# Optimization experiments

Measured on AMD Instinct MI355X. Metric: run time of the kernel, lower is better.

## Reference

```python
import jax, jax.numpy as jnp
import numpy as np

B, S, H = 2, 2048, 1024          # batch, seq, hidden_size
I = 512                          # expert_ffn_hidden_size
E_R, E_Z = 32, 8                 # routed experts, zero (identity) experts
E_T = E_R + E_Z                  # total experts
K = 6                            # moe_topk
SCALE = 2.5                      # routed_scaling_factor
W_INIT = 0.02


def setup_inputs() -> dict:
    key = jax.random.key(0)
    k0, k1, k2, k3 = jax.random.split(key, 4)
    return {
        "hidden_states": jax.random.normal(k0, (B, S, H), jnp.float32),
        "classifier_weight": jax.random.normal(k1, (E_T, H), jnp.float32) * W_INIT,
        "e_score_correction_bias": jnp.zeros((E_T,), jnp.float32),
        "gate_up_proj": jax.random.normal(k2, (E_T, 2 * I, H), jnp.float32) * W_INIT,
        "down_proj": jax.random.normal(k3, (E_R, H, I), jnp.float32) * W_INIT,
    }


def reference(hidden_states, classifier_weight, e_score_correction_bias,
              gate_up_proj, down_proj):
    orig_shape = hidden_states.shape
    x = hidden_states.reshape(-1, H).astype(jnp.float32)      # [T, H]
    T = x.shape[0]

    # ---- router (fp32 like the torch code) ----
    logits = x @ classifier_weight.T                          # [T, E_T]
    scores = jax.nn.softmax(logits, axis=-1)
    _, topk_idx = jax.lax.top_k(scores + e_score_correction_bias[None, :], K)
    topk_w = jnp.take_along_axis(scores, topk_idx, axis=1) * SCALE  # [T, K]

    # dense per-(token, expert) combine weights; 0 for unselected experts
    w_full = jnp.zeros((T, E_T), jnp.float32).at[
        jnp.arange(T)[:, None], topk_idx].add(topk_w)          # [T, E_T]

    # zero experts: weighted identity
    zero_w = w_full[:, E_R:].sum(axis=-1, keepdims=True)       # [T, 1]
    out0 = x * zero_w

    # routed experts: SwiGLU MLP per expert, scanned over experts
    routed_w = w_full[:, :E_R].T                               # [E_R, T]

    def body(out, xs):
        Wgu, Wd, we = xs                                       # [2I,H],[H,I],[T]
        gate, up = jnp.split(x @ Wgu.T, 2, axis=-1)            # [T, I] each
        y = (jax.nn.silu(gate) * up) @ Wd.T                    # [T, H]
        return out + we[:, None] * y, None

    out, _ = jax.lax.scan(body, out0, (gate_up_proj[:E_R], down_proj, routed_w))
    return out.reshape(orig_shape).astype(hidden_states.dtype)
```

## Files before the change

### kernel.cpp

```cpp
#include <hip/hip_runtime.h>
#include <float.h>
#include <math.h>

#define TT 4096
#define HH 1024
#define II 512
#define E_R 32
#define E_T 40
#define TOPK 6
#define SCALE_F 2.5f
#define MAXTILES 224
#define NGUP (32*1024*1024)
#define NDWN (32*1024*512)

typedef __bf16 bf16x8 __attribute__((ext_vector_type(8)));
typedef float f32x4 __attribute__((ext_vector_type(4)));

__device__ inline unsigned short f2bf(float f) {
  __bf16 h = (__bf16)f;
  return __builtin_bit_cast(unsigned short, h);
}

__device__ inline bf16x8 cvt8v(float4 a, float4 b) {
  bf16x8 v;
  v[0] = (__bf16)a.x; v[1] = (__bf16)a.y; v[2] = (__bf16)a.z; v[3] = (__bf16)a.w;
  v[4] = (__bf16)b.x; v[5] = (__bf16)b.y; v[6] = (__bf16)b.z; v[7] = (__bf16)b.w;
  return v;
}

__device__ inline void gload_lds16(const void* g, void* l) {
  __builtin_amdgcn_global_load_lds(
      (__attribute__((address_space(1))) void*)g,
      (__attribute__((address_space(3))) void*)l, 16, 0, 0);
}

__device__ inline bf16x8 lds_frag(const unsigned short* base, int row, int kb) {
  int byte = (row * 128 + kb * 2) ^ ((row & 7) << 4);
  uint4 v = *reinterpret_cast<const uint4*>(reinterpret_cast<const char*>(base) + byte);
  return __builtin_bit_cast(bf16x8, v);
}

__device__ inline f32x4 mfma16(bf16x8 a, bf16x8 b, f32x4 c) {
  return __builtin_amdgcn_mfma_f32_16x16x32_bf16(a, b, c, 0, 0, 0);
}

#define WAIT_VM8()  do { asm volatile("s_waitcnt vmcnt(8)" ::: "memory"); } while (0)
#define WAIT_VM0()  do { asm volatile("s_waitcnt vmcnt(0)" ::: "memory"); } while (0)
#define SBAR()      __builtin_amdgcn_s_barrier()
#define SCHED0()    __builtin_amdgcn_sched_barrier(0)

__global__ __launch_bounds__(256) void k_convert_w(const float* __restrict__ gup,
                                                   const float* __restrict__ dwn,
                                                   uint4* __restrict__ wb) {
  unsigned i = blockIdx.x * 256 + threadIdx.x;
  const unsigned NGq = NGUP / 8;
  const float4* src = (i < NGq)
      ? reinterpret_cast<const float4*>(gup) + (size_t)i * 2
      : reinterpret_cast<const float4*>(dwn) + (size_t)(i - NGq) * 2;
  float4 a = src[0], b = src[1];
  wb[i] = __builtin_bit_cast(uint4, cvt8v(a, b));
}

__global__ __launch_bounds__(256) void k_logits(const float* __restrict__ x,
                                                const float* __restrict__ wcls,
                                                float* __restrict__ logits,
                                                unsigned short* __restrict__ xb,
                                                int* __restrict__ counts) {
  __shared__ float4 ws4[E_T * 64];
  const int tid = threadIdx.x;
  const int lane = tid & 63;
  const int wave = tid >> 6;
  const int token = blockIdx.x * 4 + wave;
  if (blockIdx.x == 0 && tid < E_R) counts[tid] = 0;
  const float4* x4 = reinterpret_cast<const float4*>(x);
  const float4* w4 = reinterpret_cast<const float4*>(wcls);

  float acc[E_T];
  #pragma unroll
  for (int e = 0; e < E_T; ++e) acc[e] = 0.f;

  for (int c = 0; c < 4; ++c) {
    if (c) __syncthreads();
    #pragma unroll
    for (int j = 0; j < 10; ++j) {
      int v = tid + j * 256;
      int e = v >> 6, kq = v & 63;
      ws4[v] = w4[e * 256 + c * 64 + kq];
    }
    float4 xv = x4[(size_t)token * 256 + c * 64 + lane];
    ushort4 s;
    s.x = f2bf(xv.x); s.y = f2bf(xv.y); s.z = f2bf(xv.z); s.w = f2bf(xv.w);
    reinterpret_cast<ushort4*>(xb + (size_t)token * HH)[c * 64 + lane] = s;
    __syncthreads();
    #pragma unroll
    for (int e = 0; e < E_T; ++e) {
      float4 w = ws4[e * 64 + lane];
      acc[e] += xv.x * w.x + xv.y * w.y + xv.z * w.z + xv.w * w.w;
    }
  }

  float mine = 0.f;
  #pragma unroll
  for (int e = 0; e < E_T; ++e) {
    float r = acc[e];
    #pragma unroll
    for (int o = 32; o; o >>= 1) r += __shfl_xor(r, o);
    if (lane == e) mine = r;
  }
  if (lane < E_T) logits[(size_t)token * E_T + lane] = mine;
}

__global__ void k_topk(const float* __restrict__ logits, const float* __restrict__ bias,
                       float* __restrict__ zero_w, int* __restrict__ counts,
                       int* __restrict__ tok_list,
                       int* __restrict__ route_ep, float* __restrict__ route_w,
                       int* __restrict__ route_n) {
  int t = blockIdx.x * 64 + threadIdx.x;
  float l[E_T];
  const float4* lp = reinterpret_cast<const float4*>(logits + (size_t)t * E_T);
  #pragma unroll
  for (int j = 0; j < E_T / 4; ++j) {
    float4 v = lp[j];
    l[j * 4 + 0] = v.x; l[j * 4 + 1] = v.y; l[j * 4 + 2] = v.z; l[j * 4 + 3] = v.w;
  }
  float m = -FLT_MAX;
  #pragma unroll
  for (int e = 0; e < E_T; ++e) m = fmaxf(m, l[e]);
  float den = 0.f;
  #pragma unroll
  for (int e = 0; e < E_T; ++e) { l[e] = __expf(l[e] - m); den += l[e]; }
  float inv = 1.f / den;
  float sel[E_T];
  #pragma unroll
  for (int e = 0; e < E_T; ++e) { l[e] *= inv; sel[e] = l[e] + bias[e]; }

  unsigned long long used = 0ull;
  float zw = 0.f;
  int nr = 0;
  for (int k = 0; k < TOPK; ++k) {
    float bv = -FLT_MAX; int bj = 0;
    #pragma unroll
    for (int e = 0; e < E_T; ++e) {
      float v = ((used >> e) & 1ull) ? -FLT_MAX : sel[e];
      if (v > bv) { bv = v; bj = e; }
    }
    used |= 1ull << bj;
    float wgt = (bv - bias[bj]) * SCALE_F;
    if (bj >= E_R) {
      zw += wgt;
    } else {
      int p = atomicAdd(&counts[bj], 1);
      tok_list[bj * TT + p] = t;
      route_ep[t * TOPK + nr] = (bj << 16) | p;
      route_w[t * TOPK + nr] = wgt;
      nr++;
    }
  }
  zero_w[t] = zw;
  route_n[t] = nr;
}

__global__ void k_scan(const int* __restrict__ counts, int* __restrict__ offsets,
                       int* __restrict__ tiles) {
  if (threadIdx.x == 0) {
    int s = 0, idx = 0;
    for (int e = 0; e < E_R; ++e) {
      offsets[e] = s;
      int c = counts[e];
      s += c;
      for (int r0 = 0; r0 < c; r0 += 128) tiles[1 + idx++] = (e << 16) | r0;
    }
    offsets[E_R] = s;
    tiles[0] = idx;
  }
}

__global__ __launch_bounds__(256, 3) void k_gemm1(
    const unsigned short* __restrict__ xb, const unsigned short* __restrict__ gupb,
    const int* __restrict__ tok_list, const int* __restrict__ counts,
    const int* __restrict__ offsets, const int* __restrict__ tiles,
    unsigned short* __restrict__ inter) {
  const int nt = tiles[0];
  if ((int)blockIdx.y >= nt) return;
  const int tv = tiles[1 + blockIdx.y];
  const int e = tv >> 16;
  const int row0 = tv & 0xffff;
  const int cnt = counts[e];
  const int off = offsets[e];
  const int n0 = blockIdx.x * 64;
  const int tid = threadIdx.x;
  const int lane = tid & 63;
  const int wave = tid >> 6;
  const int wr = wave >> 1;
  const int wc = wave & 1;

  __shared__ __align__(16) unsigned short lA[2][128 * 64];
  __shared__ __align__(16) unsigned short lBg[2][64 * 64];
  __shared__ __align__(16) unsigned short lBu[2][64 * 64];
  __shared__ int toks[128];

  if (tid < 128) {
    int r = row0 + tid;
    toks[tid] = tok_list[e * TT + (r < cnt ? r : cnt - 1)];
  }
  __syncthreads();

  unsigned aoff[4];
  #pragma unroll
  for (int i = 0; i < 4; ++i) {
    int lrow = wave * 32 + i * 8 + (lane >> 3);
    aoff[i] = (unsigned)toks[lrow] * HH + (((lane & 7) ^ (lrow & 7)) * 8);
  }
  const unsigned short* gb = gupb + (size_t)e * (1024 * HH);
  unsigned boff[2];
  #pragma unroll
  for (int i = 0; i < 2; ++i) {
    int lrow = wave * 16 + i * 8 + (lane >> 3);
    boff[i] = (unsigned)(n0 + lrow) * HH + (((lane & 7) ^ (lrow & 7)) * 8);
  }
  const unsigned upjump = 512u * HH;

  f32x4 accg[4][2] = {}; f32x4 accu[4][2] = {};

#define G1_STAGE(T, B)                                                          \
  {                                                                             \
    int k0s = (T) * 64;                                                         \
    _Pragma("unroll")                                                           \
    for (int i = 0; i < 4; ++i)                                                 \
      gload_lds16(xb + aoff[i] + k0s, lA[B] + (wave * 32 + i * 8) * 64);        \
    _Pragma("unroll")                                                           \
    for (int i = 0; i < 2; ++i) {                                               \
      gload_lds16(gb + boff[i] + k0s,          lBg[B] + (wave * 16 + i * 8) * 64); \
      gload_lds16(gb + boff[i] + upjump + k0s, lBu[B] + (wave * 16 + i * 8) * 64); \
    }                                                                           \
  }

#define G1_COMPUTE(B)                                                           \
  {                                                                             \
    _Pragma("unroll")                                                           \
    for (int ks = 0; ks < 2; ++ks) {                                            \
      int kb = ks * 32 + ((lane >> 4) << 3);                                    \
      bf16x8 a[4], g[2], u[2];                                                  \
      _Pragma("unroll")                                                         \
      for (int i = 0; i < 4; ++i) a[i] = lds_frag(lA[B], wr * 64 + i * 16 + (lane & 15), kb); \
      _Pragma("unroll")                                                         \
      for (int j = 0; j < 2; ++j) {                                             \
        g[j] = lds_frag(lBg[B], wc * 32 + j * 16 + (lane & 15), kb);            \
        u[j] = lds_frag(lBu[B], wc * 32 + j * 16 + (lane & 15), kb);            \
      }                                                                         \
      _Pragma("unroll")                                                         \
      for (int i = 0; i < 4; ++i)                                               \
        _Pragma("unroll")                                                       \
        for (int j = 0; j < 2; ++j) {                                           \
          accg[i][j] = mfma16(a[i], g[j], accg[i][j]);                          \
          accu[i][j] = mfma16(a[i], u[j], accu[i][j]);                          \
        }                                                                       \
    }                                                                           \
  }

  G1_STAGE(0, 0);
  G1_STAGE(1, 1);
  WAIT_VM8();
  SBAR(); SCHED0();

  #pragma unroll 2
  for (int t = 0; t < 14; ++t) {
    if (t & 1) { G1_COMPUTE(1); } else { G1_COMPUTE(0); }
    SCHED0();
    SBAR();
    if (t & 1) { G1_STAGE(t + 2, 1); } else { G1_STAGE(t + 2, 0); }
    WAIT_VM8();
    SBAR(); SCHED0();
  }
  G1_COMPUTE(0);
  SCHED0();
  SBAR();
  WAIT_VM0();
  SBAR(); SCHED0();
  G1_COMPUTE(1);

  #pragma unroll
  for (int i = 0; i < 4; ++i)
    #pragma unroll
    for (int j = 0; j < 2; ++j)
      #pragma unroll
      for (int r = 0; r < 4; ++r) {
        int rloc = wr * 64 + i * 16 + ((lane >> 4) << 2) + r;
        int grow = row0 + rloc;
        if (grow < cnt) {
          int col = n0 + wc * 32 + j * 16 + (lane & 15);
          float gv = accg[i][j][r], uv = accu[i][j][r];
          float act = gv / (1.f + __expf(-gv)) * uv;
          inter[(size_t)(off + grow) * II + col] = f2bf(act);
        }
      }
}

__global__ __launch_bounds__(256, 3) void k_gemm2(
    const unsigned short* __restrict__ inter, const unsigned short* __restrict__ dwnb,
    const int* __restrict__ counts, const int* __restrict__ offsets,
    const int* __restrict__ tiles, unsigned short* __restrict__ inter2) {
  const int nt = tiles[0];
  if ((int)blockIdx.y >= nt) return;
  const int tv = tiles[1 + blockIdx.y];
  const int e = tv >> 16;
  const int row0 = tv & 0xffff;
  const int cnt = counts[e];
  const int off = offsets[e];
  const int h0 = blockIdx.x * 128;
  const int tid = threadIdx.x;
  const int lane = tid & 63;
  const int wave = tid >> 6;
  const int wr = wave >> 1;
  const int wc = wave & 1;

  __shared__ __align__(16) unsigned short lA[2][128 * 64];
  __shared__ __align__(16) unsigned short lB[2][128 * 64];

  unsigned aoff[4];
  #pragma unroll
  for (int i = 0; i < 4; ++i) {
    int lrow = wave * 32 + i * 8 + (lane >> 3);
    int rr = row0 + lrow; rr = rr < cnt ? rr : cnt - 1;
    aoff[i] = (unsigned)(off + rr) * II + (((lane & 7) ^ (lrow & 7)) * 8);
  }
  const unsigned short* db = dwnb + (size_t)e * (HH * II);
  unsigned boff[4];
  #pragma unroll
  for (int i = 0; i < 4; ++i) {
    int lrow = wave * 32 + i * 8 + (lane >> 3);
    boff[i] = (unsigned)(h0 + lrow) * II + (((lane & 7) ^ (lrow & 7)) * 8);
  }

  f32x4 acc[4][4] = {};

#define G2_STAGE(T, B)                                                          \
  {                                                                             \
    int k0s = (T) * 64;                                                         \
    _Pragma("unroll")                                                           \
    for (int i = 0; i < 4; ++i)                                                 \
      gload_lds16(inter + aoff[i] + k0s, lA[B] + (wave * 32 + i * 8) * 64);     \
    _Pragma("unroll")                                                           \
    for (int i = 0; i < 4; ++i)                                                 \
      gload_lds16(db + boff[i] + k0s, lB[B] + (wave * 32 + i * 8) * 64);        \
  }

#define G2_COMPUTE(B)                                                           \
  {                                                                             \
    _Pragma("unroll")                                                           \
    for (int ks = 0; ks < 2; ++ks) {                                            \
      int kb = ks * 32 + ((lane >> 4) << 3);                                    \
      bf16x8 a[4], b[4];                                                        \
      _Pragma("unroll")                                                         \
      for (int i = 0; i < 4; ++i) a[i] = lds_frag(lA[B], wr * 64 + i * 16 + (lane & 15), kb); \
      _Pragma("unroll")                                                         \
      for (int j = 0; j < 4; ++j) b[j] = lds_frag(lB[B], wc * 64 + j * 16 + (lane & 15), kb); \
      _Pragma("unroll")                                                         \
      for (int i = 0; i < 4; ++i)                                               \
        _Pragma("unroll")                                                       \
        for (int j = 0; j < 4; ++j)                                             \
          acc[i][j] = mfma16(a[i], b[j], acc[i][j]);                            \
    }                                                                           \
  }

  G2_STAGE(0, 0);
  G2_STAGE(1, 1);
  WAIT_VM8();
  SBAR(); SCHED0();

  #pragma unroll 2
  for (int t = 0; t < 6; ++t) {
    if (t & 1) { G2_COMPUTE(1); } else { G2_COMPUTE(0); }
    SCHED0();
    SBAR();
    if (t & 1) { G2_STAGE(t + 2, 1); } else { G2_STAGE(t + 2, 0); }
    WAIT_VM8();
    SBAR(); SCHED0();
  }
  G2_COMPUTE(0);
  SCHED0();
  SBAR();
  WAIT_VM0();
  SBAR(); SCHED0();
  G2_COMPUTE(1);

  #pragma unroll
  for (int i = 0; i < 4; ++i)
    #pragma unroll
    for (int j = 0; j < 4; ++j)
      #pragma unroll
      for (int r = 0; r < 4; ++r) {
        int rloc = wr * 64 + i * 16 + ((lane >> 4) << 2) + r;
        int grow = row0 + rloc;
        if (grow < cnt) {
          int h = h0 + wc * 64 + j * 16 + (lane & 15);
          inter2[(size_t)(off + grow) * HH + h] = f2bf(acc[i][j][r]);
        }
      }
}

__global__ __launch_bounds__(256) void k_combine(
    const float* __restrict__ x, const float* __restrict__ zero_w,
    const int* __restrict__ offsets, const int* __restrict__ route_ep,
    const float* __restrict__ route_w, const int* __restrict__ route_n,
    const unsigned short* __restrict__ inter2, float* __restrict__ out) {
  const int t = blockIdx.x;
  const int tid = threadIdx.x;
  const float zw = zero_w[t];
  const int n = route_n[t];
  float4 o = reinterpret_cast<const float4*>(x)[t * 256 + tid];
  o.x *= zw; o.y *= zw; o.z *= zw; o.w *= zw;
  for (int i = 0; i < n; ++i) {
    int ep = route_ep[t * TOPK + i];
    int row = offsets[ep >> 16] + (ep & 0xffff);
    float w = route_w[t * TOPK + i];
    ushort4 v = reinterpret_cast<const ushort4*>(inter2 + (size_t)row * HH)[tid];
    o.x += w * __builtin_bit_cast(float, (unsigned)v.x << 16);
    o.y += w * __builtin_bit_cast(float, (unsigned)v.y << 16);
    o.z += w * __builtin_bit_cast(float, (unsigned)v.z << 16);
    o.w += w * __builtin_bit_cast(float, (unsigned)v.w << 16);
  }
  reinterpret_cast<float4*>(out)[t * 256 + tid] = o;
}


extern "C" void kernel_launch(void* const* d_in, const int* in_sizes, int n_in,
                              void* d_out, int out_size, void* d_ws, size_t ws_size,
                              hipStream_t stream) {
  const float* x    = (const float*)d_in[0];
  const float* wcls = (const float*)d_in[1];
  const float* bias = (const float*)d_in[2];
  const float* gup  = (const float*)d_in[3];
  const float* dwn  = (const float*)d_in[4];
  float* out = (float*)d_out;

  char* w = (char*)d_ws;
  unsigned short* xb    = (unsigned short*)(w + 0);
  float* zero_w         = (float*)(w + 8388608);
  int* counts           = (int*)(w + 8404992);
  int* offsets          = (int*)(w + 8405120);
  int* tok_list         = (int*)(w + 8405376);
  float* logits         = (float*)(w + 8929664);
  int* tiles            = (int*)(w + 9585024);
  int* route_ep         = (int*)(w + 9589120);
  float* route_w        = (float*)(w + 9687424);
  int* route_n          = (int*)(w + 9785728);
  unsigned short* inter = (unsigned short*)(w + 9802112);
  unsigned short* inter2 = (unsigned short*)(w + 34967936);
  unsigned short* gupb  = (unsigned short*)(w + 85299584);
  unsigned short* dwnb  = (unsigned short*)(w + 152408448);

  k_convert_w<<<(NGUP + NDWN) / 8 / 256, 256, 0, stream>>>(gup, dwn, (uint4*)gupb);
  k_logits<<<1024, 256, 0, stream>>>(x, wcls, logits, xb, counts);
  k_topk<<<64, 64, 0, stream>>>(logits, bias, zero_w, counts, tok_list,
                                route_ep, route_w, route_n);
  k_scan<<<1, 64, 0, stream>>>(counts, offsets, tiles);
  k_gemm1<<<dim3(8, MAXTILES), 256, 0, stream>>>(xb, gupb, tok_list, counts, offsets, tiles, inter);
  k_gemm2<<<dim3(8, MAXTILES), 256, 0, stream>>>(inter, dwnb, counts, offsets, tiles, inter2);
  k_combine<<<TT, 256, 0, stream>>>(x, zero_w, offsets, route_ep, route_w, route_n,
                                    inter2, out);
}
```

Measured before the change: 247.6 us.

## Drop the separate bf16 weight conversion pass and convert fp32 weights inside the GEMMs

Removes the kernel that converted all expert gate_up and down weights to bf16 in a full read-and-write pass before the GEMMs. Both grouped GEMMs now stage the fp32 weights directly into LDS and convert them to bf16 while building the MFMA fragments. The K tile shrinks from 64 to 32 so the fp32 staging buffers fit, with new swizzles and adjusted waitcnt. In exchange, each weight tile is fetched from global memory as fp32 (twice the bytes) once per token tile of an expert, and the kernel adds extra LDS reads and conversion ALU work per fragment.

Measured after the change: 234.8 us. 5.2% less time.

```diff
diff --git a/kernel.cpp b/kernel.cpp
--- a/kernel.cpp
+++ b/kernel.cpp
@@ -10,8 +10,6 @@
 #define TOPK 6
 #define SCALE_F 2.5f
 #define MAXTILES 224
-#define NGUP (32*1024*1024)
-#define NDWN (32*1024*512)
 
 typedef __bf16 bf16x8 __attribute__((ext_vector_type(8)));
 typedef float f32x4 __attribute__((ext_vector_type(4)));
@@ -34,32 +32,30 @@
       (__attribute__((address_space(3))) void*)l, 16, 0, 0);
 }
 
-__device__ inline bf16x8 lds_frag(const unsigned short* base, int row, int kb) {
-  int byte = (row * 128 + kb * 2) ^ ((row & 7) << 4);
+__device__ inline bf16x8 lds_fragA32(const unsigned short* base, int row, int kb) {
+  int byte = row * 64 + (((kb >> 3) ^ (row & 3)) << 4);
   uint4 v = *reinterpret_cast<const uint4*>(reinterpret_cast<const char*>(base) + byte);
   return __builtin_bit_cast(bf16x8, v);
 }
 
+__device__ inline bf16x8 lds_fragB32(const float* base, int row, int kb) {
+  int key = row & 7;
+  int c0 = (kb >> 2) ^ key;
+  int c1 = ((kb >> 2) + 1) ^ key;
+  const char* p = reinterpret_cast<const char*>(base) + row * 128;
+  float4 lo = *reinterpret_cast<const float4*>(p + c0 * 16);
+  float4 hi = *reinterpret_cast<const float4*>(p + c1 * 16);
+  return cvt8v(lo, hi);
+}
+
 __device__ inline f32x4 mfma16(bf16x8 a, bf16x8 b, f32x4 c) {
   return __builtin_amdgcn_mfma_f32_16x16x32_bf16(a, b, c, 0, 0, 0);
 }
 
-#define WAIT_VM8()  do { asm volatile("s_waitcnt vmcnt(8)" ::: "memory"); } while (0)
+#define WAIT_VM6()  do { asm volatile("s_waitcnt vmcnt(6)" ::: "memory"); } while (0)
 #define WAIT_VM0()  do { asm volatile("s_waitcnt vmcnt(0)" ::: "memory"); } while (0)
 #define SBAR()      __builtin_amdgcn_s_barrier()
 #define SCHED0()    __builtin_amdgcn_sched_barrier(0)
-
-__global__ __launch_bounds__(256) void k_convert_w(const float* __restrict__ gup,
-                                                   const float* __restrict__ dwn,
-                                                   uint4* __restrict__ wb) {
-  unsigned i = blockIdx.x * 256 + threadIdx.x;
-  const unsigned NGq = NGUP / 8;
-  const float4* src = (i < NGq)
-      ? reinterpret_cast<const float4*>(gup) + (size_t)i * 2
-      : reinterpret_cast<const float4*>(dwn) + (size_t)(i - NGq) * 2;
-  float4 a = src[0], b = src[1];
-  wb[i] = __builtin_bit_cast(uint4, cvt8v(a, b));
-}
 
 __global__ __launch_bounds__(256) void k_logits(const float* __restrict__ x,
                                                 const float* __restrict__ wcls,
@@ -176,7 +172,7 @@
 }
 
 __global__ __launch_bounds__(256, 3) void k_gemm1(
-    const unsigned short* __restrict__ xb, const unsigned short* __restrict__ gupb,
+    const unsigned short* __restrict__ xb, const float* __restrict__ gup,
     const int* __restrict__ tok_list, const int* __restrict__ counts,
     const int* __restrict__ offsets, const int* __restrict__ tiles,
     unsigned short* __restrict__ inter) {
@@ -194,9 +190,9 @@
   const int wr = wave >> 1;
   const int wc = wave & 1;
 
-  __shared__ __align__(16) unsigned short lA[2][128 * 64];
-  __shared__ __align__(16) unsigned short lBg[2][64 * 64];
-  __shared__ __align__(16) unsigned short lBu[2][64 * 64];
+  __shared__ __align__(16) unsigned short lA[2][128 * 32];
+  __shared__ __align__(16) float lBg[2][64 * 32];
+  __shared__ __align__(16) float lBu[2][64 * 32];
   __shared__ int toks[128];
 
   if (tid < 128) {
@@ -205,18 +201,18 @@
   }
   __syncthreads();
 
-  unsigned aoff[4];
-  #pragma unroll
-  for (int i = 0; i < 4; ++i) {
-    int lrow = wave * 32 + i * 8 + (lane >> 3);
-    aoff[i] = (unsigned)toks[lrow] * HH + (((lane & 7) ^ (lrow & 7)) * 8);
-  }
-  const unsigned short* gb = gupb + (size_t)e * (1024 * HH);
+  unsigned aoff[2];
+  #pragma unroll
+  for (int i = 0; i < 2; ++i) {
+    int lrow = wave * 32 + i * 16 + (lane >> 2);
+    aoff[i] = (unsigned)toks[lrow] * HH + (((lane & 3) ^ (lrow & 3)) * 8);
+  }
+  const float* gbase = gup + (size_t)e * 1024 * HH;
   unsigned boff[2];
   #pragma unroll
   for (int i = 0; i < 2; ++i) {
     int lrow = wave * 16 + i * 8 + (lane >> 3);
-    boff[i] = (unsigned)(n0 + lrow) * HH + (((lane & 7) ^ (lrow & 7)) * 8);
+    boff[i] = (unsigned)(n0 + lrow) * HH + (((lane & 7) ^ (lrow & 7)) * 4);
   }
   const unsigned upjump = 512u * HH;
 
@@ -224,52 +220,49 @@
 
 #define G1_STAGE(T, B)                                                          \
   {                                                                             \
-    int k0s = (T) * 64;                                                         \
-    _Pragma("unroll")                                                           \
-    for (int i = 0; i < 4; ++i)                                                 \
-      gload_lds16(xb + aoff[i] + k0s, lA[B] + (wave * 32 + i * 8) * 64);        \
+    int k0s = (T) * 32;                                                         \
+    _Pragma("unroll")                                                           \
+    for (int i = 0; i < 2; ++i)                                                 \
+      gload_lds16(xb + aoff[i] + k0s, lA[B] + (wave * 32 + i * 16) * 32);       \
     _Pragma("unroll")                                                           \
     for (int i = 0; i < 2; ++i) {                                               \
-      gload_lds16(gb + boff[i] + k0s,          lBg[B] + (wave * 16 + i * 8) * 64); \
-      gload_lds16(gb + boff[i] + upjump + k0s, lBu[B] + (wave * 16 + i * 8) * 64); \
+      gload_lds16(gbase + boff[i] + k0s,          lBg[B] + (wave * 16 + i * 8) * 32); \
+      gload_lds16(gbase + boff[i] + upjump + k0s, lBu[B] + (wave * 16 + i * 8) * 32); \
     }                                                                           \
   }
 
 #define G1_COMPUTE(B)                                                           \
   {                                                                             \
-    _Pragma("unroll")                                                           \
-    for (int ks = 0; ks < 2; ++ks) {                                            \
-      int kb = ks * 32 + ((lane >> 4) << 3);                                    \
-      bf16x8 a[4], g[2], u[2];                                                  \
-      _Pragma("unroll")                                                         \
-      for (int i = 0; i < 4; ++i) a[i] = lds_frag(lA[B], wr * 64 + i * 16 + (lane & 15), kb); \
+    int kb = (lane >> 4) << 3;                                                  \
+    bf16x8 a[4], g[2], u[2];                                                    \
+    _Pragma("unroll")                                                           \
+    for (int i = 0; i < 4; ++i) a[i] = lds_fragA32(lA[B], wr * 64 + i * 16 + (lane & 15), kb); \
+    _Pragma("unroll")                                                           \
+    for (int j = 0; j < 2; ++j) {                                               \
+      g[j] = lds_fragB32(lBg[B], wc * 32 + j * 16 + (lane & 15), kb);           \
+      u[j] = lds_fragB32(lBu[B], wc * 32 + j * 16 + (lane & 15), kb);           \
+    }                                                                           \
+    _Pragma("unroll")                                                           \
+    for (int i = 0; i < 4; ++i)                                                 \
       _Pragma("unroll")                                                         \
       for (int j = 0; j < 2; ++j) {                                             \
-        g[j] = lds_frag(lBg[B], wc * 32 + j * 16 + (lane & 15), kb);            \
-        u[j] = lds_frag(lBu[B], wc * 32 + j * 16 + (lane & 15), kb);            \
+        accg[i][j] = mfma16(a[i], g[j], accg[i][j]);                            \
+        accu[i][j] = mfma16(a[i], u[j], accu[i][j]);                            \
       }                                                                         \
-      _Pragma("unroll")                                                         \
-      for (int i = 0; i < 4; ++i)                                               \
-        _Pragma("unroll")                                                       \
-        for (int j = 0; j < 2; ++j) {                                           \
-          accg[i][j] = mfma16(a[i], g[j], accg[i][j]);                          \
-          accu[i][j] = mfma16(a[i], u[j], accu[i][j]);                          \
-        }                                                                       \
-    }                                                                           \
   }
 
   G1_STAGE(0, 0);
   G1_STAGE(1, 1);
-  WAIT_VM8();
+  WAIT_VM6();
   SBAR(); SCHED0();
 
   #pragma unroll 2
-  for (int t = 0; t < 14; ++t) {
+  for (int t = 0; t < 30; ++t) {
     if (t & 1) { G1_COMPUTE(1); } else { G1_COMPUTE(0); }
     SCHED0();
     SBAR();
     if (t & 1) { G1_STAGE(t + 2, 1); } else { G1_STAGE(t + 2, 0); }
-    WAIT_VM8();
+    WAIT_VM6();
     SBAR(); SCHED0();
   }
   G1_COMPUTE(0);
@@ -297,7 +290,7 @@
 }
 
 __global__ __launch_bounds__(256, 3) void k_gemm2(
-    const unsigned short* __restrict__ inter, const unsigned short* __restrict__ dwnb,
+    const unsigned short* __restrict__ inter, const float* __restrict__ dwn,
     const int* __restrict__ counts, const int* __restrict__ offsets,
     const int* __restrict__ tiles, unsigned short* __restrict__ inter2) {
   const int nt = tiles[0];
@@ -314,67 +307,64 @@
   const int wr = wave >> 1;
   const int wc = wave & 1;
 
-  __shared__ __align__(16) unsigned short lA[2][128 * 64];
-  __shared__ __align__(16) unsigned short lB[2][128 * 64];
-
-  unsigned aoff[4];
+  __shared__ __align__(16) unsigned short lA[2][128 * 32];
+  __shared__ __align__(16) float lB[2][128 * 32];
+
+  unsigned aoff[2];
+  #pragma unroll
+  for (int i = 0; i < 2; ++i) {
+    int lrow = wave * 32 + i * 16 + (lane >> 2);
+    int rr = row0 + lrow; rr = rr < cnt ? rr : cnt - 1;
+    aoff[i] = (unsigned)(off + rr) * II + (((lane & 3) ^ (lrow & 3)) * 8);
+  }
+  const float* dbase = dwn + (size_t)e * HH * II;
+  unsigned boff[4];
   #pragma unroll
   for (int i = 0; i < 4; ++i) {
     int lrow = wave * 32 + i * 8 + (lane >> 3);
-    int rr = row0 + lrow; rr = rr < cnt ? rr : cnt - 1;
-    aoff[i] = (unsigned)(off + rr) * II + (((lane & 7) ^ (lrow & 7)) * 8);
-  }
-  const unsigned short* db = dwnb + (size_t)e * (HH * II);
-  unsigned boff[4];
-  #pragma unroll
-  for (int i = 0; i < 4; ++i) {
-    int lrow = wave * 32 + i * 8 + (lane >> 3);
-    boff[i] = (unsigned)(h0 + lrow) * II + (((lane & 7) ^ (lrow & 7)) * 8);
+    boff[i] = (unsigned)(h0 + lrow) * II + (((lane & 7) ^ (lrow & 7)) * 4);
   }
 
   f32x4 acc[4][4] = {};
 
 #define G2_STAGE(T, B)                                                          \
   {                                                                             \
-    int k0s = (T) * 64;                                                         \
+    int k0s = (T) * 32;                                                         \
+    _Pragma("unroll")                                                           \
+    for (int i = 0; i < 2; ++i)                                                 \
+      gload_lds16(inter + aoff[i] + k0s, lA[B] + (wave * 32 + i * 16) * 32);    \
     _Pragma("unroll")                                                           \
     for (int i = 0; i < 4; ++i)                                                 \
-      gload_lds16(inter + aoff[i] + k0s, lA[B] + (wave * 32 + i * 8) * 64);     \
-    _Pragma("unroll")                                                           \
-    for (int i = 0; i < 4; ++i)                                                 \
-      gload_lds16(db + boff[i] + k0s, lB[B] + (wave * 32 + i * 8) * 64);        \
+      gload_lds16(dbase + boff[i] + k0s, lB[B] + (wave * 32 + i * 8) * 32);     \
   }
 
 #define G2_COMPUTE(B)                                                           \
   {                                                                             \
-    _Pragma("unroll")                                                           \
-    for (int ks = 0; ks < 2; ++ks) {                                            \
-      int kb = ks * 32 + ((lane >> 4) << 3);                                    \
-      bf16x8 a[4], b[4];                                                        \
+    int kb = (lane >> 4) << 3;                                                  \
+    bf16x8 a[4], b[4];                                                          \
+    _Pragma("unroll")                                                           \
+    for (int i = 0; i < 4; ++i) a[i] = lds_fragA32(lA[B], wr * 64 + i * 16 + (lane & 15), kb); \
+    _Pragma("unroll")                                                           \
+    for (int j = 0; j < 4; ++j) b[j] = lds_fragB32(lB[B], wc * 64 + j * 16 + (lane & 15), kb); \
+    _Pragma("unroll")                                                           \
+    for (int i = 0; i < 4; ++i)                                                 \
       _Pragma("unroll")                                                         \
-      for (int i = 0; i < 4; ++i) a[i] = lds_frag(lA[B], wr * 64 + i * 16 + (lane & 15), kb); \
-      _Pragma("unroll")                                                         \
-      for (int j = 0; j < 4; ++j) b[j] = lds_frag(lB[B], wc * 64 + j * 16 + (lane & 15), kb); \
-      _Pragma("unroll")                                                         \
-      for (int i = 0; i < 4; ++i)                                               \
-        _Pragma("unroll")                                                       \
-        for (int j = 0; j < 4; ++j)                                             \
-          acc[i][j] = mfma16(a[i], b[j], acc[i][j]);                            \
-    }                                                                           \
+      for (int j = 0; j < 4; ++j)                                               \
+        acc[i][j] = mfma16(a[i], b[j], acc[i][j]);                              \
   }
 
   G2_STAGE(0, 0);
   G2_STAGE(1, 1);
-  WAIT_VM8();
+  WAIT_VM6();
   SBAR(); SCHED0();
 
   #pragma unroll 2
-  for (int t = 0; t < 6; ++t) {
+  for (int t = 0; t < 14; ++t) {
     if (t & 1) { G2_COMPUTE(1); } else { G2_COMPUTE(0); }
     SCHED0();
     SBAR();
     if (t & 1) { G2_STAGE(t + 2, 1); } else { G2_STAGE(t + 2, 0); }
-    WAIT_VM8();
+    WAIT_VM6();
     SBAR(); SCHED0();
   }
   G2_COMPUTE(0);
@@ -447,16 +437,13 @@
   int* route_n          = (int*)(w + 9785728);
   unsigned short* inter = (unsigned short*)(w + 9802112);
   unsigned short* inter2 = (unsigned short*)(w + 34967936);
-  unsigned short* gupb  = (unsigned short*)(w + 85299584);
-  unsigned short* dwnb  = (unsigned short*)(w + 152408448);
-
-  k_convert_w<<<(NGUP + NDWN) / 8 / 256, 256, 0, stream>>>(gup, dwn, (uint4*)gupb);
+
   k_logits<<<1024, 256, 0, stream>>>(x, wcls, logits, xb, counts);
   k_topk<<<64, 64, 0, stream>>>(logits, bias, zero_w, counts, tok_list,
                                 route_ep, route_w, route_n);
   k_scan<<<1, 64, 0, stream>>>(counts, offsets, tiles);
-  k_gemm1<<<dim3(8, MAXTILES), 256, 0, stream>>>(xb, gupb, tok_list, counts, offsets, tiles, inter);
-  k_gemm2<<<dim3(8, MAXTILES), 256, 0, stream>>>(inter, dwnb, counts, offsets, tiles, inter2);
+  k_gemm1<<<dim3(8, MAXTILES), 256, 0, stream>>>(xb, gup, tok_list, counts, offsets, tiles, inter);
+  k_gemm2<<<dim3(8, MAXTILES), 256, 0, stream>>>(inter, dwn, counts, offsets, tiles, inter2);
   k_combine<<<TT, 256, 0, stream>>>(x, zero_w, offsets, route_ep, route_w, route_n,
                                     inter2, out);
 }
```

## Fuse fp32-to-bf16 weight conversion into grouped GEMM LDS fragment loads

Applied to the files above, without the earlier changes.

Drops the separate kernel that converted all expert weights to bf16 on every call. The GEMMs now stream fp32 weights straight into LDS with a new 16-way XOR swizzle and convert to bf16 when reading fragments for the MFMA. The A operand becomes single-buffered and is loaded one step ahead instead of two. This avoids a full read and write of the weight tensors each call. In exchange each GEMM tile reads twice the weight bytes from global memory, doubles LDS use for B, and adds per-fragment conversion work.

New measurement: 241.9 us. -2.3%, faster.

```diff
diff --git a/kernel.cpp b/kernel.cpp
--- a/kernel.cpp
+++ b/kernel.cpp
@@ -10,8 +10,6 @@
 #define TOPK 6
 #define SCALE_F 2.5f
 #define MAXTILES 224
-#define NGUP (32*1024*1024)
-#define NDWN (32*1024*512)
 
 typedef __bf16 bf16x8 __attribute__((ext_vector_type(8)));
 typedef float f32x4 __attribute__((ext_vector_type(4)));
@@ -40,6 +38,16 @@
   return __builtin_bit_cast(bf16x8, v);
 }
 
+__device__ inline bf16x8 lds_frag_f32(const float* base, int row, int kb) {
+  int key = row & 15;
+  int c0 = (kb >> 2) ^ key;
+  int c1 = ((kb >> 2) + 1) ^ key;
+  const char* p = reinterpret_cast<const char*>(base) + row * 256;
+  float4 lo = *reinterpret_cast<const float4*>(p + c0 * 16);
+  float4 hi = *reinterpret_cast<const float4*>(p + c1 * 16);
+  return cvt8v(lo, hi);
+}
+
 __device__ inline f32x4 mfma16(bf16x8 a, bf16x8 b, f32x4 c) {
   return __builtin_amdgcn_mfma_f32_16x16x32_bf16(a, b, c, 0, 0, 0);
 }
@@ -48,18 +56,6 @@
 #define WAIT_VM0()  do { asm volatile("s_waitcnt vmcnt(0)" ::: "memory"); } while (0)
 #define SBAR()      __builtin_amdgcn_s_barrier()
 #define SCHED0()    __builtin_amdgcn_sched_barrier(0)
-
-__global__ __launch_bounds__(256) void k_convert_w(const float* __restrict__ gup,
-                                                   const float* __restrict__ dwn,
-                                                   uint4* __restrict__ wb) {
-  unsigned i = blockIdx.x * 256 + threadIdx.x;
-  const unsigned NGq = NGUP / 8;
-  const float4* src = (i < NGq)
-      ? reinterpret_cast<const float4*>(gup) + (size_t)i * 2
-      : reinterpret_cast<const float4*>(dwn) + (size_t)(i - NGq) * 2;
-  float4 a = src[0], b = src[1];
-  wb[i] = __builtin_bit_cast(uint4, cvt8v(a, b));
-}
 
 __global__ __launch_bounds__(256) void k_logits(const float* __restrict__ x,
                                                 const float* __restrict__ wcls,
@@ -176,7 +172,7 @@
 }
 
 __global__ __launch_bounds__(256, 3) void k_gemm1(
-    const unsigned short* __restrict__ xb, const unsigned short* __restrict__ gupb,
+    const unsigned short* __restrict__ xb, const float* __restrict__ gup,
     const int* __restrict__ tok_list, const int* __restrict__ counts,
     const int* __restrict__ offsets, const int* __restrict__ tiles,
     unsigned short* __restrict__ inter) {
@@ -194,59 +190,53 @@
   const int wr = wave >> 1;
   const int wc = wave & 1;
 
-  __shared__ __align__(16) unsigned short lA[2][128 * 64];
-  __shared__ __align__(16) unsigned short lBg[2][64 * 64];
-  __shared__ __align__(16) unsigned short lBu[2][64 * 64];
-  __shared__ int toks[128];
-
-  if (tid < 128) {
-    int r = row0 + tid;
-    toks[tid] = tok_list[e * TT + (r < cnt ? r : cnt - 1)];
-  }
-  __syncthreads();
+  __shared__ __align__(16) unsigned short lA[128 * 64];
+  __shared__ __align__(16) float lBg[2][64 * 64];
+  __shared__ __align__(16) float lBu[2][64 * 64];
 
   unsigned aoff[4];
   #pragma unroll
   for (int i = 0; i < 4; ++i) {
     int lrow = wave * 32 + i * 8 + (lane >> 3);
-    aoff[i] = (unsigned)toks[lrow] * HH + (((lane & 7) ^ (lrow & 7)) * 8);
-  }
-  const unsigned short* gb = gupb + (size_t)e * (1024 * HH);
-  unsigned boff[2];
-  #pragma unroll
-  for (int i = 0; i < 2; ++i) {
-    int lrow = wave * 16 + i * 8 + (lane >> 3);
-    boff[i] = (unsigned)(n0 + lrow) * HH + (((lane & 7) ^ (lrow & 7)) * 8);
+    int rr = row0 + lrow; rr = rr < cnt ? rr : cnt - 1;
+    aoff[i] = (unsigned)tok_list[e * TT + rr] * HH + (((lane & 7) ^ (lrow & 7)) * 8);
+  }
+  const float* gbase = gup + (size_t)e * 1024 * HH;
+  unsigned boff[4];
+  #pragma unroll
+  for (int i = 0; i < 4; ++i) {
+    int rt = wave * 16 + i * 4 + (lane >> 4);
+    boff[i] = (unsigned)(n0 + rt) * HH + (((lane & 15) ^ (rt & 15)) * 4);
   }
   const unsigned upjump = 512u * HH;
 
   f32x4 accg[4][2] = {}; f32x4 accu[4][2] = {};
 
-#define G1_STAGE(T, B)                                                          \
-  {                                                                             \
-    int k0s = (T) * 64;                                                         \
+#define G1_STAGE_A(T)                                                           \
+  { int k0s = (T) * 64;                                                         \
     _Pragma("unroll")                                                           \
     for (int i = 0; i < 4; ++i)                                                 \
-      gload_lds16(xb + aoff[i] + k0s, lA[B] + (wave * 32 + i * 8) * 64);        \
+      gload_lds16(xb + aoff[i] + k0s, lA + (wave * 32 + i * 8) * 64); }
+
+#define G1_STAGE_B(T, B)                                                        \
+  { int k0s = (T) * 64;                                                         \
     _Pragma("unroll")                                                           \
-    for (int i = 0; i < 2; ++i) {                                               \
-      gload_lds16(gb + boff[i] + k0s,          lBg[B] + (wave * 16 + i * 8) * 64); \
-      gload_lds16(gb + boff[i] + upjump + k0s, lBu[B] + (wave * 16 + i * 8) * 64); \
-    }                                                                           \
-  }
+    for (int i = 0; i < 4; ++i) {                                               \
+      gload_lds16(gbase + boff[i] + k0s,          lBg[B] + (wave * 16 + i * 4) * 64); \
+      gload_lds16(gbase + boff[i] + upjump + k0s, lBu[B] + (wave * 16 + i * 4) * 64); \
+    } }
 
 #define G1_COMPUTE(B)                                                           \
-  {                                                                             \
-    _Pragma("unroll")                                                           \
+  { _Pragma("unroll")                                                           \
     for (int ks = 0; ks < 2; ++ks) {                                            \
       int kb = ks * 32 + ((lane >> 4) << 3);                                    \
       bf16x8 a[4], g[2], u[2];                                                  \
       _Pragma("unroll")                                                         \
-      for (int i = 0; i < 4; ++i) a[i] = lds_frag(lA[B], wr * 64 + i * 16 + (lane & 15), kb); \
+      for (int i = 0; i < 4; ++i) a[i] = lds_frag(lA, wr * 64 + i * 16 + (lane & 15), kb); \
       _Pragma("unroll")                                                         \
       for (int j = 0; j < 2; ++j) {                                             \
-        g[j] = lds_frag(lBg[B], wc * 32 + j * 16 + (lane & 15), kb);            \
-        u[j] = lds_frag(lBu[B], wc * 32 + j * 16 + (lane & 15), kb);            \
+        g[j] = lds_frag_f32(lBg[B], wc * 32 + j * 16 + (lane & 15), kb);        \
+        u[j] = lds_frag_f32(lBu[B], wc * 32 + j * 16 + (lane & 15), kb);        \
       }                                                                         \
       _Pragma("unroll")                                                         \
       for (int i = 0; i < 4; ++i)                                               \
@@ -255,11 +245,11 @@
           accg[i][j] = mfma16(a[i], g[j], accg[i][j]);                          \
           accu[i][j] = mfma16(a[i], u[j], accu[i][j]);                          \
         }                                                                       \
-    }                                                                           \
-  }
-
-  G1_STAGE(0, 0);
-  G1_STAGE(1, 1);
+    } }
+
+  G1_STAGE_A(0);
+  G1_STAGE_B(0, 0);
+  G1_STAGE_B(1, 1);
   WAIT_VM8();
   SBAR(); SCHED0();
 
@@ -268,13 +258,14 @@
     if (t & 1) { G1_COMPUTE(1); } else { G1_COMPUTE(0); }
     SCHED0();
     SBAR();
-    if (t & 1) { G1_STAGE(t + 2, 1); } else { G1_STAGE(t + 2, 0); }
+    G1_STAGE_A(t + 1);
+    if (t & 1) { G1_STAGE_B(t + 2, 1); } else { G1_STAGE_B(t + 2, 0); }
     WAIT_VM8();
     SBAR(); SCHED0();
   }
   G1_COMPUTE(0);
-  SCHED0();
-  SBAR();
+  SCHED0(); SBAR();
+  G1_STAGE_A(15);
   WAIT_VM0();
   SBAR(); SCHED0();
   G1_COMPUTE(1);
@@ -297,7 +288,7 @@
 }
 
 __global__ __launch_bounds__(256, 3) void k_gemm2(
-    const unsigned short* __restrict__ inter, const unsigned short* __restrict__ dwnb,
+    const unsigned short* __restrict__ inter, const float* __restrict__ dwn,
     const int* __restrict__ counts, const int* __restrict__ offsets,
     const int* __restrict__ tiles, unsigned short* __restrict__ inter2) {
   const int nt = tiles[0];
@@ -314,8 +305,8 @@
   const int wr = wave >> 1;
   const int wc = wave & 1;
 
-  __shared__ __align__(16) unsigned short lA[2][128 * 64];
-  __shared__ __align__(16) unsigned short lB[2][128 * 64];
+  __shared__ __align__(16) unsigned short lA[128 * 64];
+  __shared__ __align__(16) float lB[2][128 * 64];
 
   unsigned aoff[4];
   #pragma unroll
@@ -324,47 +315,47 @@
     int rr = row0 + lrow; rr = rr < cnt ? rr : cnt - 1;
     aoff[i] = (unsigned)(off + rr) * II + (((lane & 7) ^ (lrow & 7)) * 8);
   }
-  const unsigned short* db = dwnb + (size_t)e * (HH * II);
-  unsigned boff[4];
-  #pragma unroll
-  for (int i = 0; i < 4; ++i) {
-    int lrow = wave * 32 + i * 8 + (lane >> 3);
-    boff[i] = (unsigned)(h0 + lrow) * II + (((lane & 7) ^ (lrow & 7)) * 8);
+  const float* dbase = dwn + (size_t)e * HH * II;
+  unsigned boff[8];
+  #pragma unroll
+  for (int i = 0; i < 8; ++i) {
+    int rt = wave * 32 + i * 4 + (lane >> 4);
+    boff[i] = (unsigned)(h0 + rt) * II + (((lane & 15) ^ (rt & 15)) * 4);
   }
 
   f32x4 acc[4][4] = {};
 
-#define G2_STAGE(T, B)                                                          \
-  {                                                                             \
-    int k0s = (T) * 64;                                                         \
+#define G2_STAGE_A(T)                                                           \
+  { int k0s = (T) * 64;                                                         \
     _Pragma("unroll")                                                           \
     for (int i = 0; i < 4; ++i)                                                 \
-      gload_lds16(inter + aoff[i] + k0s, lA[B] + (wave * 32 + i * 8) * 64);     \
+      gload_lds16(inter + aoff[i] + k0s, lA + (wave * 32 + i * 8) * 64); }
+
+#define G2_STAGE_B(T, B)                                                        \
+  { int k0s = (T) * 64;                                                         \
     _Pragma("unroll")                                                           \
-    for (int i = 0; i < 4; ++i)                                                 \
-      gload_lds16(db + boff[i] + k0s, lB[B] + (wave * 32 + i * 8) * 64);        \
-  }
+    for (int i = 0; i < 8; ++i)                                                 \
+      gload_lds16(dbase + boff[i] + k0s, lB[B] + (wave * 32 + i * 4) * 64); }
 
 #define G2_COMPUTE(B)                                                           \
-  {                                                                             \
-    _Pragma("unroll")                                                           \
+  { _Pragma("unroll")                                                           \
     for (int ks = 0; ks < 2; ++ks) {                                            \
       int kb = ks * 32 + ((lane >> 4) << 3);                                    \
       bf16x8 a[4], b[4];                                                        \
       _Pragma("unroll")                                                         \
-      for (int i = 0; i < 4; ++i) a[i] = lds_frag(lA[B], wr * 64 + i * 16 + (lane & 15), kb); \
-      _Pragma("unroll")                                                         \
-      for (int j = 0; j < 4; ++j) b[j] = lds_frag(lB[B], wc * 64 + j * 16 + (lane & 15), kb); \
+      for (int i = 0; i < 4; ++i) a[i] = lds_frag(lA, wr * 64 + i * 16 + (lane & 15), kb); \
+      _Pragma("unroll")                                                         \
+      for (int j = 0; j < 4; ++j) b[j] = lds_frag_f32(lB[B], wc * 64 + j * 16 + (lane & 15), kb); \
       _Pragma("unroll")                                                         \
       for (int i = 0; i < 4; ++i)                                               \
         _Pragma("unroll")                                                       \
         for (int j = 0; j < 4; ++j)                                             \
           acc[i][j] = mfma16(a[i], b[j], acc[i][j]);                            \
-    }                                                                           \
-  }
-
-  G2_STAGE(0, 0);
-  G2_STAGE(1, 1);
+    } }
+
+  G2_STAGE_A(0);
+  G2_STAGE_B(0, 0);
+  G2_STAGE_B(1, 1);
   WAIT_VM8();
   SBAR(); SCHED0();
 
@@ -373,13 +364,14 @@
     if (t & 1) { G2_COMPUTE(1); } else { G2_COMPUTE(0); }
     SCHED0();
     SBAR();
-    if (t & 1) { G2_STAGE(t + 2, 1); } else { G2_STAGE(t + 2, 0); }
+    G2_STAGE_A(t + 1);
+    if (t & 1) { G2_STAGE_B(t + 2, 1); } else { G2_STAGE_B(t + 2, 0); }
     WAIT_VM8();
     SBAR(); SCHED0();
   }
   G2_COMPUTE(0);
-  SCHED0();
-  SBAR();
+  SCHED0(); SBAR();
+  G2_STAGE_A(7);
   WAIT_VM0();
   SBAR(); SCHED0();
   G2_COMPUTE(1);
@@ -447,16 +439,13 @@
   int* route_n          = (int*)(w + 9785728);
   unsigned short* inter = (unsigned short*)(w + 9802112);
   unsigned short* inter2 = (unsigned short*)(w + 34967936);
-  unsigned short* gupb  = (unsigned short*)(w + 85299584);
-  unsigned short* dwnb  = (unsigned short*)(w + 152408448);
-
-  k_convert_w<<<(NGUP + NDWN) / 8 / 256, 256, 0, stream>>>(gup, dwn, (uint4*)gupb);
+
   k_logits<<<1024, 256, 0, stream>>>(x, wcls, logits, xb, counts);
   k_topk<<<64, 64, 0, stream>>>(logits, bias, zero_w, counts, tok_list,
                                 route_ep, route_w, route_n);
   k_scan<<<1, 64, 0, stream>>>(counts, offsets, tiles);
-  k_gemm1<<<dim3(8, MAXTILES), 256, 0, stream>>>(xb, gupb, tok_list, counts, offsets, tiles, inter);
-  k_gemm2<<<dim3(8, MAXTILES), 256, 0, stream>>>(inter, dwnb, counts, offsets, tiles, inter2);
+  k_gemm1<<<dim3(8, MAXTILES), 256, 0, stream>>>(xb, gup, tok_list, counts, offsets, tiles, inter);
+  k_gemm2<<<dim3(8, MAXTILES), 256, 0, stream>>>(inter, dwn, counts, offsets, tiles, inter2);
   k_combine<<<TT, 256, 0, stream>>>(x, zero_w, offsets, route_ep, route_w, route_n,
                                     inter2, out);
 }
```
